# Optimization experiments

Hardware: AMD Instinct MI355X
Metric: run time of the kernel (lower is better)

Reference implementation:

```python
import jax, jax.numpy as jnp
import numpy as np

AMP = 2  # from init_kwargs

def setup_inputs() -> dict:
    key = jax.random.key(0)
    k1, k2 = jax.random.split(key)
    B, C, H, W = 4, 32, 256, 256
    x_q = jax.random.normal(k1, (B, C, H, W), dtype=jnp.float32)
    x_k = jax.random.normal(k2, (B, C, H, W), dtype=jnp.float32)
    return {"x_q": x_q, "x_k": x_k, "num_heads": 4}


def reference(x_q, x_k, num_heads):
    amp = AMP
    ks = 2 * amp + 1  # kernel_size
    B, C, H, W = x_q.shape
    head_dim = C // num_heads
    scale = head_dim ** (-0.5)
    # (B, head_dim, heads, H, W)
    q = x_q.reshape(B, head_dim, num_heads, H, W) * scale
    k = x_k.reshape(B, head_dim, num_heads, H, W)
    k_pad = jnp.pad(k, ((0, 0), (0, 0), (0, 0), (amp, amp), (amp, amp)))
    # validity mask: padded region is invalid (mask < 0.5 in original)
    valid = jnp.pad(jnp.ones((H, W), dtype=x_q.dtype), ((amp, amp), (amp, amp)))
    attn = []
    for i in range(ks):  # static loop over 25 offsets
        for j in range(ks):
            # per-offset dot product over head_dim -> (B, heads, H, W)
            a = jnp.sum(q * k_pad[:, :, :, i:i + H, j:j + W], axis=1)
            a = jnp.where(valid[i:i + H, j:j + W] > 0.5, a, jnp.asarray(-1000.0, a.dtype))
            attn.append(a)
    attn = jnp.stack(attn, axis=1)          # (B, ks*ks, heads, H, W)
    attn = jax.nn.softmax(attn, axis=1)
    # offset grid: arange(-s//2+1, s//2+1) == [-amp, ..., amp]
    offs = jnp.arange(-amp, amp + 1, dtype=x_q.dtype)
    grid = jnp.stack(jnp.meshgrid(offs, offs, indexing='ij'), axis=-1).reshape(ks * ks, 2)
    # offset-weighted sum over the ks*ks window positions -> (B, 2, heads, H, W)
    v_ = jnp.einsum('bkhxy,kc->bchxy', attn, grid)
    # mean over heads -> (B, 2, H, W)
    return jnp.mean(v_, axis=2)
```

## Files before the change

kernel.cpp:

```cpp
#include <hip/hip_runtime.h>

#define Bdim 4
#define Cdim 32
#define NH   4
#define HD   8
#define Hdim 256
#define Wdim 256
#define AMP  2
#define KS   5

#define XT    32
#define TY    4
#define TROWS 8
#define TPOS  40
#define NPAIRS 16
#define PAIR_STRIDE (TROWS * TPOS)
#define TILE_SLOTS (NPAIRS * PAIR_STRIDE)

typedef _Float16 h2 __attribute__((ext_vector_type(2)));

static __device__ __forceinline__ float dot2acc(h2 a, h2 b, float c) {
#if __has_builtin(__builtin_amdgcn_fdot2)
    return __builtin_amdgcn_fdot2(a, b, c, false);
#else
    return c + (float)a.x * (float)b.x + (float)a.y * (float)b.y;
#endif
}

__global__ __launch_bounds__(256) void natt_offset_kernel(
    const float* __restrict__ xq,
    const float* __restrict__ xk,
    float* __restrict__ out)
{
    __shared__ __align__(16) float kt[TILE_SLOTS];

    const int tid = threadIdx.x;
    const int bid = blockIdx.x;
    const int r8  = bid & 7;
    const int u   = bid >> 3;
    const int yt  = r8 * 8 + (u & 7);
    const int rst = u >> 3;
    const int xt  = rst & 7;
    const int b   = rst >> 3;

    const int Y0 = yt * TY;
    const int X0 = xt * XT;
    const bool interior = (yt != 0) && (yt != 63) && (xt != 0) && (xt != 7);

    const int h    = tid >> 6;
    const int lane = tid & 63;
    const int row  = lane >> 4;
    const int qx   = lane & 15;
    const int y    = Y0 + row;
    const int x0   = X0 + qx * 2;

    const size_t plane = (size_t)Hdim * Wdim;
    const float scale = 0.35355339059327373f;

    {
        const float* kb = xk + (size_t)b * Cdim * plane;
        if (interior) {
            #pragma unroll
            for (int it = 0; it < 5; ++it) {
                const int j = lane + it * 64;
                const int c4 = j % 10;
                const int t  = j / 10;
                const int rw = t % TROWS;
                const int d2 = t / TROWS;
                const int c0 = 8 * d2 + h;
                const int yr = Y0 - AMP + rw;
                const int xs = X0 - 6 + c4 * 4;
                const float* pa = kb + (size_t)c0 * plane + (size_t)yr * Wdim + xs;
                const float4 va = *(const float4*)pa;
                const float4 vb = *(const float4*)(pa + 4 * plane);
                const float a[4]  = {va.x, va.y, va.z, va.w};
                const float bb[4] = {vb.x, vb.y, vb.z, vb.w};
                float o[4];
                #pragma unroll
                for (int k2 = 0; k2 < 4; ++k2) {
                    h2 pk;
                    pk.x = (_Float16)a[k2];
                    pk.y = (_Float16)bb[k2];
                    o[k2] = __builtin_bit_cast(float, pk);
                }
                *(float4*)(kt + ((d2 << 2) | h) * PAIR_STRIDE + rw * TPOS + c4 * 4) =
                    make_float4(o[0], o[1], o[2], o[3]);
            }
        } else {
            #pragma unroll
            for (int it = 0; it < 5; ++it) {
                const int j = lane + it * 64;
                const int c4 = j % 10;
                const int t  = j / 10;
                const int rw = t % TROWS;
                const int d2 = t / TROWS;
                const int c0 = 8 * d2 + h;
                int yr = Y0 - AMP + rw;
                yr = yr < 0 ? 0 : (yr > Hdim - 1 ? Hdim - 1 : yr);
                const int xs = X0 - 6 + c4 * 4;
                const int xc = xs < 0 ? 0 : (xs > Wdim - 4 ? Wdim - 4 : xs);
                const int sh = xs - xc;
                const float* pa = kb + (size_t)c0 * plane + (size_t)yr * Wdim + xc;
                const float4 va = *(const float4*)pa;
                const float4 vb = *(const float4*)(pa + 4 * plane);
                const float a[4]  = {va.x, va.y, va.z, va.w};
                const float bb[4] = {vb.x, vb.y, vb.z, vb.w};
                float o[4];
                #pragma unroll
                for (int k2 = 0; k2 < 4; ++k2) {
                    int idx = k2 + sh;
                    idx = idx < 0 ? 0 : (idx > 3 ? 3 : idx);
                    h2 pk;
                    pk.x = (_Float16)a[idx];
                    pk.y = (_Float16)bb[idx];
                    o[k2] = __builtin_bit_cast(float, pk);
                }
                *(float4*)(kt + ((d2 << 2) | h) * PAIR_STRIDE + rw * TPOS + c4 * 4) =
                    make_float4(o[0], o[1], o[2], o[3]);
            }
        }
    }

    const float* qb = xq + (size_t)b * Cdim * plane + (size_t)y * Wdim + x0;
    h2 q2[4][2];
    #pragma unroll
    for (int d2 = 0; d2 < 4; ++d2) {
        const float2 qa = *(const float2*)(qb + (size_t)((2 * d2)     * NH + h) * plane);
        const float2 qc = *(const float2*)(qb + (size_t)((2 * d2 + 1) * NH + h) * plane);
        const float qa2[2] = {qa.x, qa.y};
        const float qc2[2] = {qc.x, qc.y};
        #pragma unroll
        for (int p = 0; p < 2; ++p) {
            q2[d2][p].x = (_Float16)(qa2[p] * scale);
            q2[d2][p].y = (_Float16)(qc2[p] * scale);
        }
    }


    float Z[2]  = {0.f, 0.f};
    float sx[2] = {0.f, 0.f};
    float sy[2] = {0.f, 0.f};

    #pragma unroll
    for (int r = 0; r < KS; ++r) {
        float dot[KS][2];
        #pragma unroll
        for (int dj = 0; dj < KS; ++dj) { dot[dj][0] = 0.f; dot[dj][1] = 0.f; }

        #pragma unroll
        for (int d2 = 0; d2 < 4; ++d2) {
            const float* wp = kt + ((d2 << 2) | h) * PAIR_STRIDE
                                 + (row + r) * TPOS + (qx * 2 + 4);
            const float2 wa = *(const float2*)wp;
            const float2 wb = *(const float2*)(wp + 2);
            const float2 wc = *(const float2*)(wp + 4);
            const float wf[6] = {wa.x, wa.y, wb.x, wb.y, wc.x, wc.y};
            h2 w[6];
            #pragma unroll
            for (int k2 = 0; k2 < 6; ++k2) w[k2] = __builtin_bit_cast(h2, wf[k2]);
            #pragma unroll
            for (int dj = 0; dj < KS; ++dj) {
                #pragma unroll
                for (int p = 0; p < 2; ++p)
                    dot[dj][p] = dot2acc(q2[d2][p], w[p + dj], dot[dj][p]);
            }
        }

        const float fdi = (float)(r - AMP);
        if (interior) {
            #pragma unroll
            for (int p = 0; p < 2; ++p) {
                float e[KS];
                #pragma unroll
                for (int dj = 0; dj < KS; ++dj) e[dj] = __expf(dot[dj][p]);
                const float er = ((e[0] + e[1]) + (e[2] + e[3])) + e[4];
                Z[p]  += er;
                sx[p] += fdi * er;
                sy[p] += (e[3] - e[1]) + 2.f * (e[4] - e[0]);
            }
        } else {
            const int yy = y + r - AMP;
            const bool rowok = (yy >= 0) && (yy < Hdim);
            #pragma unroll
            for (int p = 0; p < 2; ++p) {
                float e[KS];
                #pragma unroll
                for (int dj = 0; dj < KS; ++dj) {
                    const int xx = x0 + p + dj - AMP;
                    const bool ok = rowok && (xx >= 0) && (xx < Wdim);
                    e[dj] = ok ? __expf(dot[dj][p]) : 0.f;
                }
                const float er = ((e[0] + e[1]) + (e[2] + e[3])) + e[4];
                Z[p]  += er;
                sx[p] += fdi * er;
                sy[p] += (e[3] - e[1]) + 2.f * (e[4] - e[0]);
            }
        }
    }

    __syncthreads();
    float* red = kt;
    const int pxl = row * XT + qx * 2;
    {
        const float i0 = 1.f / Z[0], i1 = 1.f / Z[1];
        *(float2*)(red + (h * 2 + 0) * (XT * TY) + pxl) =
            make_float2(sx[0]*i0, sx[1]*i1);
        *(float2*)(red + (h * 2 + 1) * (XT * TY) + pxl) =
            make_float2(sy[0]*i0, sy[1]*i1);
    }
    __syncthreads();

    if (h < 2) {
        float acc[2] = {0.f, 0.f};
        #pragma unroll
        for (int hh = 0; hh < NH; ++hh) {
            const float2 v = *(const float2*)(red + (hh * 2 + h) * (XT * TY) + pxl);
            acc[0] += v.x; acc[1] += v.y;
        }
        *(float2*)(out + ((size_t)b * 2 + h) * plane + (size_t)y * Wdim + x0) =
            make_float2(acc[0]*0.25f, acc[1]*0.25f);
    }
}

extern "C" void kernel_launch(void* const* d_in, const int* in_sizes, int n_in,
                              void* d_out, int out_size, void* d_ws, size_t ws_size,
                              hipStream_t stream) {
    const float* xq = (const float*)d_in[0];
    const float* xk = (const float*)d_in[1];
    float* out = (float*)d_out;

    natt_offset_kernel<<<dim3(2048, 1, 1), dim3(256, 1, 1), 0, stream>>>(xq, xk, out);
}
```

Baseline: 101.6 us.

## Software-pipeline per-channel-pair key staging with dot-product compute

The key-tile staging is split into four stages, one per channel pair. The global loads for the next pair are issued while the current pair's dot products are computed from LDS. Dot accumulators are restructured into a 5x5x2 array held across all pairs, and softmax accumulation moves after all pairs are done. Launch bounds gain a minimum-blocks hint of 4. The aim is to hide global-load latency behind compute, at the cost of more live registers and fewer loads in flight at once.

```diff
diff --git a/kernel.cpp b/kernel.cpp
--- a/kernel.cpp
+++ b/kernel.cpp
@@ -27,7 +27,7 @@
 #endif
 }
 
-__global__ __launch_bounds__(256) void natt_offset_kernel(
+__global__ __launch_bounds__(256, 4) void natt_offset_kernel(
     const float* __restrict__ xq,
     const float* __restrict__ xk,
     float* __restrict__ out)
@@ -57,70 +57,6 @@
     const size_t plane = (size_t)Hdim * Wdim;
     const float scale = 0.35355339059327373f;
 
-    {
-        const float* kb = xk + (size_t)b * Cdim * plane;
-        if (interior) {
-            #pragma unroll
-            for (int it = 0; it < 5; ++it) {
-                const int j = lane + it * 64;
-                const int c4 = j % 10;
-                const int t  = j / 10;
-                const int rw = t % TROWS;
-                const int d2 = t / TROWS;
-                const int c0 = 8 * d2 + h;
-                const int yr = Y0 - AMP + rw;
-                const int xs = X0 - 6 + c4 * 4;
-                const float* pa = kb + (size_t)c0 * plane + (size_t)yr * Wdim + xs;
-                const float4 va = *(const float4*)pa;
-                const float4 vb = *(const float4*)(pa + 4 * plane);
-                const float a[4]  = {va.x, va.y, va.z, va.w};
-                const float bb[4] = {vb.x, vb.y, vb.z, vb.w};
-                float o[4];
-                #pragma unroll
-                for (int k2 = 0; k2 < 4; ++k2) {
-                    h2 pk;
-                    pk.x = (_Float16)a[k2];
-                    pk.y = (_Float16)bb[k2];
-                    o[k2] = __builtin_bit_cast(float, pk);
-                }
-                *(float4*)(kt + ((d2 << 2) | h) * PAIR_STRIDE + rw * TPOS + c4 * 4) =
-                    make_float4(o[0], o[1], o[2], o[3]);
-            }
-        } else {
-            #pragma unroll
-            for (int it = 0; it < 5; ++it) {
-                const int j = lane + it * 64;
-                const int c4 = j % 10;
-                const int t  = j / 10;
-                const int rw = t % TROWS;
-                const int d2 = t / TROWS;
-                const int c0 = 8 * d2 + h;
-                int yr = Y0 - AMP + rw;
-                yr = yr < 0 ? 0 : (yr > Hdim - 1 ? Hdim - 1 : yr);
-                const int xs = X0 - 6 + c4 * 4;
-                const int xc = xs < 0 ? 0 : (xs > Wdim - 4 ? Wdim - 4 : xs);
-                const int sh = xs - xc;
-                const float* pa = kb + (size_t)c0 * plane + (size_t)yr * Wdim + xc;
-                const float4 va = *(const float4*)pa;
-                const float4 vb = *(const float4*)(pa + 4 * plane);
-                const float a[4]  = {va.x, va.y, va.z, va.w};
-                const float bb[4] = {vb.x, vb.y, vb.z, vb.w};
-                float o[4];
-                #pragma unroll
-                for (int k2 = 0; k2 < 4; ++k2) {
-                    int idx = k2 + sh;
-                    idx = idx < 0 ? 0 : (idx > 3 ? 3 : idx);
-                    h2 pk;
-                    pk.x = (_Float16)a[idx];
-                    pk.y = (_Float16)bb[idx];
-                    o[k2] = __builtin_bit_cast(float, pk);
-                }
-                *(float4*)(kt + ((d2 << 2) | h) * PAIR_STRIDE + rw * TPOS + c4 * 4) =
-                    make_float4(o[0], o[1], o[2], o[3]);
-            }
-        }
-    }
-
     const float* qb = xq + (size_t)b * Cdim * plane + (size_t)y * Wdim + x0;
     h2 q2[4][2];
     #pragma unroll
@@ -136,19 +72,75 @@
         }
     }
 
-
-    float Z[2]  = {0.f, 0.f};
-    float sx[2] = {0.f, 0.f};
-    float sy[2] = {0.f, 0.f};
-
+    const float* kb = xk + (size_t)b * Cdim * plane;
+
+    const int c4_0 = lane % 10,        rw_0 = lane / 10;
+    const int c4_1 = (64 + lane) % 10, rw_1 = (64 + lane) / 10;
+    int yr0 = Y0 - AMP + rw_0, yr1 = Y0 - AMP + rw_1;
+    int xs0 = X0 - 6 + c4_0 * 4, xs1 = X0 - 6 + c4_1 * 4;
+    int sh0 = 0, sh1 = 0;
+    if (!interior) {
+        yr0 = yr0 < 0 ? 0 : (yr0 > Hdim - 1 ? Hdim - 1 : yr0);
+        yr1 = yr1 < 0 ? 0 : (yr1 > Hdim - 1 ? Hdim - 1 : yr1);
+        int xc0 = xs0 < 0 ? 0 : (xs0 > Wdim - 4 ? Wdim - 4 : xs0);
+        int xc1 = xs1 < 0 ? 0 : (xs1 > Wdim - 4 ? Wdim - 4 : xs1);
+        sh0 = xs0 - xc0; xs0 = xc0;
+        sh1 = xs1 - xc1; xs1 = xc1;
+    }
+    const size_t off0 = (size_t)yr0 * Wdim + xs0;
+    const size_t off1 = (size_t)yr1 * Wdim + xs1;
+
+    float4 A0, B0, A1, B1;
+
+    auto stage_load = [&](int d2) {
+        const float* pa = kb + (size_t)(8 * d2 + h) * plane + off0;
+        A0 = *(const float4*)pa;
+        B0 = *(const float4*)(pa + 4 * plane);
+        if (lane < 16) {
+            const float* pb = kb + (size_t)(8 * d2 + h) * plane + off1;
+            A1 = *(const float4*)pb;
+            B1 = *(const float4*)(pb + 4 * plane);
+        }
+    };
+    auto stage_write = [&](int d2) {
+        const int base = ((d2 << 2) | h) * PAIR_STRIDE;
+        {
+            const float a[4]  = {A0.x, A0.y, A0.z, A0.w};
+            const float bb[4] = {B0.x, B0.y, B0.z, B0.w};
+            float o[4];
+            #pragma unroll
+            for (int k2 = 0; k2 < 4; ++k2) {
+                int idx = k2 + sh0; idx = idx < 0 ? 0 : (idx > 3 ? 3 : idx);
+                h2 pk; pk.x = (_Float16)a[idx]; pk.y = (_Float16)bb[idx];
+                o[k2] = __builtin_bit_cast(float, pk);
+            }
+            *(float4*)(kt + base + rw_0 * TPOS + c4_0 * 4) =
+                make_float4(o[0], o[1], o[2], o[3]);
+        }
+        if (lane < 16) {
+            const float a[4]  = {A1.x, A1.y, A1.z, A1.w};
+            const float bb[4] = {B1.x, B1.y, B1.z, B1.w};
+            float o[4];
+            #pragma unroll
+            for (int k2 = 0; k2 < 4; ++k2) {
+                int idx = k2 + sh1; idx = idx < 0 ? 0 : (idx > 3 ? 3 : idx);
+                h2 pk; pk.x = (_Float16)a[idx]; pk.y = (_Float16)bb[idx];
+                o[k2] = __builtin_bit_cast(float, pk);
+            }
+            *(float4*)(kt + base + rw_1 * TPOS + c4_1 * 4) =
+                make_float4(o[0], o[1], o[2], o[3]);
+        }
+    };
+
+    float dot[KS][KS][2];
     #pragma unroll
-    for (int r = 0; r < KS; ++r) {
-        float dot[KS][2];
-        #pragma unroll
-        for (int dj = 0; dj < KS; ++dj) { dot[dj][0] = 0.f; dot[dj][1] = 0.f; }
-
-        #pragma unroll
-        for (int d2 = 0; d2 < 4; ++d2) {
+    for (int r = 0; r < KS; ++r)
+        #pragma unroll
+        for (int dj = 0; dj < KS; ++dj) { dot[r][dj][0] = 0.f; dot[r][dj][1] = 0.f; }
+
+    auto compute_pair = [&](int d2) {
+        #pragma unroll
+        for (int r = 0; r < KS; ++r) {
             const float* wp = kt + ((d2 << 2) | h) * PAIR_STRIDE
                                  + (row + r) * TPOS + (qx * 2 + 4);
             const float2 wa = *(const float2*)wp;
@@ -162,17 +154,37 @@
             for (int dj = 0; dj < KS; ++dj) {
                 #pragma unroll
                 for (int p = 0; p < 2; ++p)
-                    dot[dj][p] = dot2acc(q2[d2][p], w[p + dj], dot[dj][p]);
-            }
-        }
-
+                    dot[r][dj][p] = dot2acc(q2[d2][p], w[p + dj], dot[r][dj][p]);
+            }
+        }
+    };
+
+    stage_load(0);
+    stage_write(0);
+    stage_load(1);
+    compute_pair(0);
+    stage_write(1);
+    stage_load(2);
+    compute_pair(1);
+    stage_write(2);
+    stage_load(3);
+    compute_pair(2);
+    stage_write(3);
+    compute_pair(3);
+
+    float Z[2]  = {0.f, 0.f};
+    float sx[2] = {0.f, 0.f};
+    float sy[2] = {0.f, 0.f};
+
+    #pragma unroll
+    for (int r = 0; r < KS; ++r) {
         const float fdi = (float)(r - AMP);
         if (interior) {
             #pragma unroll
             for (int p = 0; p < 2; ++p) {
                 float e[KS];
                 #pragma unroll
-                for (int dj = 0; dj < KS; ++dj) e[dj] = __expf(dot[dj][p]);
+                for (int dj = 0; dj < KS; ++dj) e[dj] = __expf(dot[r][dj][p]);
                 const float er = ((e[0] + e[1]) + (e[2] + e[3])) + e[4];
                 Z[p]  += er;
                 sx[p] += fdi * er;
@@ -188,7 +200,7 @@
                 for (int dj = 0; dj < KS; ++dj) {
                     const int xx = x0 + p + dj - AMP;
                     const bool ok = rowok && (xx >= 0) && (xx < Wdim);
-                    e[dj] = ok ? __expf(dot[dj][p]) : 0.f;
+                    e[dj] = ok ? __expf(dot[r][dj][p]) : 0.f;
                 }
                 const float er = ((e[0] + e[1]) + (e[2] + e[3])) + e[4];
                 Z[p]  += er;
```

Result: slower. 127.0 us (+25.0%).

## Double tile height to 8 rows with 512-thread blocks sharing the K halo

Applied to the files above, without the earlier changes.

Each block now covers 8 output rows instead of 4 and runs 512 threads in two row groups per head. All threads cooperatively stage a 12-row K halo into shared memory, so halo rows are re-read less often (12 rows loaded per 8 outputs instead of 8 per 4). A barrier is added after staging because threads now read rows loaded by other wavefronts. The boundary shift select is also rewritten as explicit cases. The grid is halved, which raises shared memory per block and could reduce the number of resident blocks.

```diff
diff --git a/kernel.cpp b/kernel.cpp
--- a/kernel.cpp
+++ b/kernel.cpp
@@ -10,12 +10,13 @@
 #define KS   5
 
 #define XT    32
-#define TY    4
-#define TROWS 8
+#define TY    8
+#define TROWS 12
 #define TPOS  40
 #define NPAIRS 16
 #define PAIR_STRIDE (TROWS * TPOS)
 #define TILE_SLOTS (NPAIRS * PAIR_STRIDE)
+#define NJOBS (NPAIRS * TROWS * 10)
 
 typedef _Float16 h2 __attribute__((ext_vector_type(2)));
 
@@ -27,7 +28,7 @@
 #endif
 }
 
-__global__ __launch_bounds__(256) void natt_offset_kernel(
+__global__ __launch_bounds__(512) void natt_offset_kernel(
     const float* __restrict__ xq,
     const float* __restrict__ xk,
     float* __restrict__ out)
@@ -38,20 +39,22 @@
     const int bid = blockIdx.x;
     const int r8  = bid & 7;
     const int u   = bid >> 3;
-    const int yt  = r8 * 8 + (u & 7);
-    const int rst = u >> 3;
+    const int yt  = r8 * 4 + (u & 3);
+    const int rst = u >> 2;
     const int xt  = rst & 7;
     const int b   = rst >> 3;
 
     const int Y0 = yt * TY;
     const int X0 = xt * XT;
-    const bool interior = (yt != 0) && (yt != 63) && (xt != 0) && (xt != 7);
-
-    const int h    = tid >> 6;
+    const bool interior = (yt != 0) && (yt != 31) && (xt != 0) && (xt != 7);
+
+    const int w    = tid >> 6;
+    const int h    = w & 3;
+    const int wrb  = (w >> 2) * 4;
     const int lane = tid & 63;
     const int row  = lane >> 4;
     const int qx   = lane & 15;
-    const int y    = Y0 + row;
+    const int y    = Y0 + wrb + row;
     const int x0   = X0 + qx * 2;
 
     const size_t plane = (size_t)Hdim * Wdim;
@@ -61,62 +64,68 @@
         const float* kb = xk + (size_t)b * Cdim * plane;
         if (interior) {
             #pragma unroll
-            for (int it = 0; it < 5; ++it) {
-                const int j = lane + it * 64;
-                const int c4 = j % 10;
-                const int t  = j / 10;
-                const int rw = t % TROWS;
-                const int d2 = t / TROWS;
-                const int c0 = 8 * d2 + h;
-                const int yr = Y0 - AMP + rw;
-                const int xs = X0 - 6 + c4 * 4;
-                const float* pa = kb + (size_t)c0 * plane + (size_t)yr * Wdim + xs;
-                const float4 va = *(const float4*)pa;
-                const float4 vb = *(const float4*)(pa + 4 * plane);
-                const float a[4]  = {va.x, va.y, va.z, va.w};
-                const float bb[4] = {vb.x, vb.y, vb.z, vb.w};
-                float o[4];
-                #pragma unroll
-                for (int k2 = 0; k2 < 4; ++k2) {
-                    h2 pk;
-                    pk.x = (_Float16)a[k2];
-                    pk.y = (_Float16)bb[k2];
-                    o[k2] = __builtin_bit_cast(float, pk);
+            for (int it = 0; it < 4; ++it) {
+                const int j = tid + it * 512;
+                if (j < NJOBS) {
+                    const int c4 = j % 10;
+                    const int t  = j / 10;
+                    const int rw = t % TROWS;
+                    const int p  = t / TROWS;
+                    const int c0 = 8 * (p >> 2) + (p & 3);
+                    const int yr = Y0 - AMP + rw;
+                    const int xs = X0 - 6 + c4 * 4;
+                    const float* pa = kb + (size_t)c0 * plane + (size_t)yr * Wdim + xs;
+                    const float4 va = *(const float4*)pa;
+                    const float4 vb = *(const float4*)(pa + 4 * plane);
+                    const float a[4]  = {va.x, va.y, va.z, va.w};
+                    const float bb[4] = {vb.x, vb.y, vb.z, vb.w};
+                    float o[4];
+                    #pragma unroll
+                    for (int k2 = 0; k2 < 4; ++k2) {
+                        h2 pk;
+                        pk.x = (_Float16)a[k2];
+                        pk.y = (_Float16)bb[k2];
+                        o[k2] = __builtin_bit_cast(float, pk);
+                    }
+                    *(float4*)(kt + p * PAIR_STRIDE + rw * TPOS + c4 * 4) =
+                        make_float4(o[0], o[1], o[2], o[3]);
                 }
-                *(float4*)(kt + ((d2 << 2) | h) * PAIR_STRIDE + rw * TPOS + c4 * 4) =
-                    make_float4(o[0], o[1], o[2], o[3]);
             }
         } else {
             #pragma unroll
-            for (int it = 0; it < 5; ++it) {
-                const int j = lane + it * 64;
-                const int c4 = j % 10;
-                const int t  = j / 10;
-                const int rw = t % TROWS;
-                const int d2 = t / TROWS;
-                const int c0 = 8 * d2 + h;
-                int yr = Y0 - AMP + rw;
-                yr = yr < 0 ? 0 : (yr > Hdim - 1 ? Hdim - 1 : yr);
-                const int xs = X0 - 6 + c4 * 4;
-                const int xc = xs < 0 ? 0 : (xs > Wdim - 4 ? Wdim - 4 : xs);
-                const int sh = xs - xc;
-                const float* pa = kb + (size_t)c0 * plane + (size_t)yr * Wdim + xc;
-                const float4 va = *(const float4*)pa;
-                const float4 vb = *(const float4*)(pa + 4 * plane);
-                const float a[4]  = {va.x, va.y, va.z, va.w};
-                const float bb[4] = {vb.x, vb.y, vb.z, vb.w};
-                float o[4];
-                #pragma unroll
-                for (int k2 = 0; k2 < 4; ++k2) {
-                    int idx = k2 + sh;
-                    idx = idx < 0 ? 0 : (idx > 3 ? 3 : idx);
-                    h2 pk;
-                    pk.x = (_Float16)a[idx];
-                    pk.y = (_Float16)bb[idx];
-                    o[k2] = __builtin_bit_cast(float, pk);
+            for (int it = 0; it < 4; ++it) {
+                const int j = tid + it * 512;
+                if (j < NJOBS) {
+                    const int c4 = j % 10;
+                    const int t  = j / 10;
+                    const int rw = t % TROWS;
+                    const int p  = t / TROWS;
+                    const int c0 = 8 * (p >> 2) + (p & 3);
+                    int yr = Y0 - AMP + rw;
+                    yr = yr < 0 ? 0 : (yr > Hdim - 1 ? Hdim - 1 : yr);
+                    const int xs = X0 - 6 + c4 * 4;
+                    const int xc = xs < 0 ? 0 : (xs > Wdim - 4 ? Wdim - 4 : xs);
+                    const int sh = xs - xc;
+                    const float* pa = kb + (size_t)c0 * plane + (size_t)yr * Wdim + xc;
+                    const float4 va = *(const float4*)pa;
+                    const float4 vb = *(const float4*)(pa + 4 * plane);
+                    const float a[4]  = {va.x, va.y, va.z, va.w};
+                    const float bb[4] = {vb.x, vb.y, vb.z, vb.w};
+                    float o[4];
+                    #pragma unroll
+                    for (int k2 = 0; k2 < 4; ++k2) {
+                        const int ip2 = (k2 + 2 > 3) ? 3 : k2 + 2;
+                        const int im2 = (k2 - 2 < 0) ? 0 : k2 - 2;
+                        const float fa = sh == 0 ? a[k2]
+                                       : (sh == 2 ? a[ip2] : (sh == -2 ? a[im2] : a[0]));
+                        const float fb = sh == 0 ? bb[k2]
+                                       : (sh == 2 ? bb[ip2] : (sh == -2 ? bb[im2] : bb[0]));
+                        h2 pk; pk.x = (_Float16)fa; pk.y = (_Float16)fb;
+                        o[k2] = __builtin_bit_cast(float, pk);
+                    }
+                    *(float4*)(kt + p * PAIR_STRIDE + rw * TPOS + c4 * 4) =
+                        make_float4(o[0], o[1], o[2], o[3]);
                 }
-                *(float4*)(kt + ((d2 << 2) | h) * PAIR_STRIDE + rw * TPOS + c4 * 4) =
-                    make_float4(o[0], o[1], o[2], o[3]);
             }
         }
     }
@@ -136,6 +145,7 @@
         }
     }
 
+    __syncthreads();
 
     float Z[2]  = {0.f, 0.f};
     float sx[2] = {0.f, 0.f};
@@ -150,19 +160,19 @@
         #pragma unroll
         for (int d2 = 0; d2 < 4; ++d2) {
             const float* wp = kt + ((d2 << 2) | h) * PAIR_STRIDE
-                                 + (row + r) * TPOS + (qx * 2 + 4);
+                                 + (wrb + row + r) * TPOS + (qx * 2 + 4);
             const float2 wa = *(const float2*)wp;
             const float2 wb = *(const float2*)(wp + 2);
             const float2 wc = *(const float2*)(wp + 4);
             const float wf[6] = {wa.x, wa.y, wb.x, wb.y, wc.x, wc.y};
-            h2 w[6];
-            #pragma unroll
-            for (int k2 = 0; k2 < 6; ++k2) w[k2] = __builtin_bit_cast(h2, wf[k2]);
+            h2 wreg[6];
+            #pragma unroll
+            for (int k2 = 0; k2 < 6; ++k2) wreg[k2] = __builtin_bit_cast(h2, wf[k2]);
             #pragma unroll
             for (int dj = 0; dj < KS; ++dj) {
                 #pragma unroll
                 for (int p = 0; p < 2; ++p)
-                    dot[dj][p] = dot2acc(q2[d2][p], w[p + dj], dot[dj][p]);
+                    dot[dj][p] = dot2acc(q2[d2][p], wreg[p + dj], dot[dj][p]);
             }
         }
 
@@ -200,7 +210,7 @@
 
     __syncthreads();
     float* red = kt;
-    const int pxl = row * XT + qx * 2;
+    const int pxl = (wrb + row) * XT + qx * 2;
     {
         const float i0 = 1.f / Z[0], i1 = 1.f / Z[1];
         *(float2*)(red + (h * 2 + 0) * (XT * TY) + pxl) =
@@ -210,14 +220,17 @@
     }
     __syncthreads();
 
-    if (h < 2) {
+    if (w < 4) {
+        const int ch  = w & 1;
+        const int rr  = (w >> 1) * 4 + row;
+        const int px2 = rr * XT + qx * 2;
         float acc[2] = {0.f, 0.f};
         #pragma unroll
         for (int hh = 0; hh < NH; ++hh) {
-            const float2 v = *(const float2*)(red + (hh * 2 + h) * (XT * TY) + pxl);
+            const float2 v = *(const float2*)(red + (hh * 2 + ch) * (XT * TY) + px2);
             acc[0] += v.x; acc[1] += v.y;
         }
-        *(float2*)(out + ((size_t)b * 2 + h) * plane + (size_t)y * Wdim + x0) =
+        *(float2*)(out + ((size_t)b * 2 + ch) * plane + (size_t)(Y0 + rr) * Wdim + x0) =
             make_float2(acc[0]*0.25f, acc[1]*0.25f);
     }
 }
@@ -229,5 +242,5 @@
     const float* xk = (const float*)d_in[1];
     float* out = (float*)d_out;
 
-    natt_offset_kernel<<<dim3(2048, 1, 1), dim3(256, 1, 1), 0, stream>>>(xq, xk, out);
+    natt_offset_kernel<<<dim3(1024, 1, 1), dim3(512, 1, 1), 0, stream>>>(xq, xk, out);
 }
```

Result: no change. 100.1 us, median of 2 (-1.5%).
